# Kernel tuning notes

Hardware: AMD Instinct MI355X
Metric: run time of the kernel (lower is better)

Reference implementation:

```python
import jax, jax.numpy as jnp
import numpy as np

DIM = 1024


def _combine(e1, e2):
    # associative op for h_t = a_t * h_{t-1} + b_t (inclusive scan, h_0-contrib handled outside)
    a1, b1 = e1
    a2, b2 = e2
    return a1 * a2, b2 + a2 * b1


def setup_inputs() -> dict:
    key = jax.random.key(0)
    ks = jax.random.split(key, 11)
    s = 1.0 / np.sqrt(DIM)
    d = {
        "x": jax.random.normal(ks[0], (4, 4096, DIM), jnp.float32),
        "hidden": jax.random.normal(ks[1], (4, DIM), jnp.float32),
        "Wf": jax.random.uniform(ks[2], (DIM, DIM), jnp.float32, -s, s),
        "bf": jax.random.uniform(ks[3], (DIM,), jnp.float32, -s, s),
        "Wi": jax.random.uniform(ks[4], (DIM, DIM), jnp.float32, -s, s),
        "bi": jax.random.uniform(ks[5], (DIM,), jnp.float32, -s, s),
        "Wig": jax.random.uniform(ks[6], (DIM, DIM), jnp.float32, -s, s),
        "big": jax.random.uniform(ks[7], (DIM,), jnp.float32, -s, s),
        "Wog": jax.random.uniform(ks[8], (DIM, DIM), jnp.float32, -s, s),
        "bog": jax.random.uniform(ks[9], (DIM,), jnp.float32, -s, s),
    }
    return d


def reference(x, hidden, Wf, bf, Wi, bi, Wig, big, Wog, bog):
    # x: [B, L, D], hidden: [B, D]
    forget = jax.nn.sigmoid(jnp.einsum("bld,ed->ble", x, Wf) + bf)
    inp = jnp.tanh(jnp.einsum("bld,ed->ble", x, Wi) + bi) * \
          jax.nn.sigmoid(jnp.einsum("bld,ed->ble", x, Wig) + big)
    # parallel scan of h_t = forget_t * h_{t-1} + inp_t with h_0 = 0
    _, h_inner = jax.lax.associative_scan(_combine, (forget, inp), axis=1)
    # add initial-hidden contribution: hidden * prod_{s<=t} forget_s
    h = h_inner + hidden[:, None, :] * jnp.cumprod(forget, axis=1)
    y = jnp.tanh(h) * jax.nn.sigmoid(jnp.einsum("bld,ed->ble", x, Wog) + bog)
    return y, h[:, -1, :]
```

## Files before the change

### kernel.cpp

```cpp
#include <hip/hip_runtime.h>
#include <hip/hip_bf16.h>
#include <cstdint>
#include <cstddef>

#define DIMD 1024
#define LSEQ 4096
#define BATCH 4
#define MTOT (BATCH*LSEQ)
#define NCHUNK 64
#define CHUNKLEN 64
#define GATE_ELEMS ((size_t)MTOT*DIMD)
#define NTILE_K 32

typedef __bf16 bf16x8 __attribute__((ext_vector_type(8)));
typedef float f32x4 __attribute__((ext_vector_type(4)));

__device__ __forceinline__ unsigned short f2bf(float f) {
    union { float f; uint32_t u; } v; v.f = f;
    uint32_t r = v.u + 0x7fffu + ((v.u >> 16) & 1u);
    return (unsigned short)(r >> 16);
}
__device__ __forceinline__ float bits2f(unsigned short b) {
    union { uint32_t u; float f; } v; v.u = ((uint32_t)b) << 16; return v.f;
}
__device__ __forceinline__ float gld(const float* p, size_t o) { return p[o]; }
__device__ __forceinline__ float gld(const unsigned short* p, size_t o) { return bits2f(p[o]); }
__device__ __forceinline__ void  gst(float* p, size_t o, float v) { p[o] = v; }
__device__ __forceinline__ void  gst(unsigned short* p, size_t o, float v) { p[o] = f2bf(v); }

__device__ __forceinline__ float fsig(float x) {
    return __builtin_amdgcn_rcpf(1.f + __expf(-x));
}

__global__ void cast_all(const float* __restrict__ x,
                         const float* __restrict__ Wf, const float* __restrict__ Wi,
                         const float* __restrict__ Wig, const float* __restrict__ Wog,
                         unsigned short* __restrict__ Xb, unsigned short* __restrict__ Wcat) {
    int b = blockIdx.x;
    const float* src; unsigned short* dst; int lb;
    if (b < 8192) { src = x; dst = Xb; lb = b; }
    else {
        int w = (b - 8192) >> 9;
        lb = (b - 8192) & 511;
        src = (w == 0) ? Wf : (w == 1) ? Wi : (w == 2) ? Wig : Wog;
        dst = Wcat + (size_t)w * DIMD * DIMD;
    }
    int i = (lb * 256 + threadIdx.x) * 8;
    float4 a = *(const float4*)(src + i);
    float4 c = *(const float4*)(src + i + 4);
    uint4 o;
    o.x = (uint32_t)f2bf(a.x) | ((uint32_t)f2bf(a.y) << 16);
    o.y = (uint32_t)f2bf(a.z) | ((uint32_t)f2bf(a.w) << 16);
    o.z = (uint32_t)f2bf(c.x) | ((uint32_t)f2bf(c.y) << 16);
    o.w = (uint32_t)f2bf(c.z) | ((uint32_t)f2bf(c.w) << 16);
    *(uint4*)(dst + i) = o;
}

template <typename T>
__global__ __launch_bounds__(512, 4) void gemm_gates_s(
    const unsigned short* __restrict__ Xb,
    const unsigned short* __restrict__ Wcat,
    const float* __restrict__ bf_, const float* __restrict__ bi_,
    const float* __restrict__ big_, const float* __restrict__ bog_,
    T* __restrict__ G)
{
    __shared__ __align__(16) char lds[73728];
    char* ldsA = lds;
    char* ldsB = lds + 24576;

    const int tid = threadIdx.x;
    const int wave = tid >> 6, lane = tid & 63;
    const int wm = wave >> 2, wn = wave & 3;
    const int l15 = lane & 15, l4 = lane >> 4;

    const int wg = blockIdx.x;
    const int swz = (wg & 7) * 256 + (wg >> 3);
    const int mt = swz & 127, nt = swz >> 7;
    const int m0 = mt * 128, n0 = nt * 256;

    const int rsw = (l4 ^ ((l15 >> 1) & 3)) << 4;
    const char* ArdBase = ldsA + (wm * 64 + l15) * 64 + rsw;
    const char* BrdBase = ldsB + (wn * 64 + l15) * 64 + rsw;

    const int srow = tid >> 2;
    const int scg  = ((tid & 3) ^ ((srow >> 1) & 3)) * 8;
    const unsigned short* pAsrc  = Xb   + (size_t)(m0 + srow) * DIMD + scg;
    const unsigned short* pBsrc0 = Wcat + (size_t)(n0 + srow) * DIMD + scg;
    const unsigned short* pBsrc1 = Wcat + (size_t)(n0 + 128 + srow) * DIMD + scg;

    auto stage3 = [&](int k0, int offA, int offB) {
        __builtin_amdgcn_global_load_lds(
            (const __attribute__((address_space(1))) uint32_t*)(pAsrc + k0),
            (__attribute__((address_space(3))) uint32_t*)(ldsA + offA + (wave << 10)), 16, 0, 0);
        __builtin_amdgcn_global_load_lds(
            (const __attribute__((address_space(1))) uint32_t*)(pBsrc0 + k0),
            (__attribute__((address_space(3))) uint32_t*)(ldsB + offB + (wave << 10)), 16, 0, 0);
        __builtin_amdgcn_global_load_lds(
            (const __attribute__((address_space(1))) uint32_t*)(pBsrc1 + k0),
            (__attribute__((address_space(3))) uint32_t*)(ldsB + offB + 8192 + (wave << 10)), 16, 0, 0);
    };

    f32x4 acc[4][4];
#pragma unroll
    for (int m = 0; m < 4; ++m)
#pragma unroll
        for (int n = 0; n < 4; ++n) acc[m][n] = (f32x4)0.f;

    stage3(0, 0, 0);
    stage3(32, 8192, 16384);

    int offA0 = 0, offA1 = 8192, offA2 = 16384;
    int offB0 = 0, offB1 = 16384, offB2 = 32768;
#pragma unroll 1
    for (int t = 0; t < NTILE_K; ++t) {
        if (t <= NTILE_K - 2) asm volatile("s_waitcnt vmcnt(3)" ::: "memory");
        else                  asm volatile("s_waitcnt vmcnt(0)" ::: "memory");
        __builtin_amdgcn_s_barrier();
        __builtin_amdgcn_sched_barrier(0);

        if (t + 2 < NTILE_K) stage3((t + 2) * 32, offA2, offB2);

        bf16x8 bv[4], avl[2], avh[2];
#pragma unroll
        for (int n = 0; n < 4; ++n)
            bv[n] = *(const bf16x8*)(BrdBase + offB0 + n * 1024);
        avl[0] = *(const bf16x8*)(ArdBase + offA0);
        avl[1] = *(const bf16x8*)(ArdBase + offA0 + 1024);

        __builtin_amdgcn_s_setprio(1);
#pragma unroll
        for (int m = 0; m < 2; ++m)
#pragma unroll
            for (int n = 0; n < 4; ++n)
                acc[m][n] = __builtin_amdgcn_mfma_f32_16x16x32_bf16(avl[m], bv[n], acc[m][n], 0, 0, 0);
        __builtin_amdgcn_s_setprio(0);

        avh[0] = *(const bf16x8*)(ArdBase + offA0 + 2048);
        avh[1] = *(const bf16x8*)(ArdBase + offA0 + 3072);

        __builtin_amdgcn_s_setprio(1);
#pragma unroll
        for (int m = 0; m < 2; ++m)
#pragma unroll
            for (int n = 0; n < 4; ++n)
                acc[2 + m][n] = __builtin_amdgcn_mfma_f32_16x16x32_bf16(avh[m], bv[n], acc[2 + m][n], 0, 0, 0);
        __builtin_amdgcn_s_setprio(0);

        int ta = offA0; offA0 = offA1; offA1 = offA2; offA2 = ta;
        int tb = offB0; offB0 = offB1; offB1 = offB2; offB2 = tb;
    }

    const int gate = n0 >> 10;
    const float* bias = (gate == 0) ? bf_ : (gate == 1) ? bi_ : (gate == 2) ? big_ : bog_;
    T* Gg = G + (size_t)gate * GATE_ELEMS;
    const int ebase = (n0 & 1023) + wn * 64;
    const int rowb0 = m0 + wm * 64;
    float bvv[4];
#pragma unroll
    for (int nf = 0; nf < 4; ++nf) bvv[nf] = bias[ebase + nf * 16 + l15];
#pragma unroll
    for (int mf = 0; mf < 4; ++mf) {
        int rowb = rowb0 + mf * 16 + l4 * 4;
#pragma unroll
        for (int r = 0; r < 4; ++r) {
            size_t rowoff = (size_t)(rowb + r) * DIMD;
#pragma unroll
            for (int nf = 0; nf < 4; ++nf) {
                float pre = acc[mf][nf][r] + bvv[nf];
                float v = (gate == 1) ? (2.f * fsig(2.f * pre) - 1.f) : fsig(pre);
                gst(Gg, rowoff + ebase + nf * 16 + l15, v);
            }
        }
    }
}

template <typename T>
__global__ void scan_phase1(const T* __restrict__ F, const T* __restrict__ TI,
                            const T* __restrict__ SG,
                            float* __restrict__ Aagg, float* __restrict__ Bagg) {
    const int d = blockIdx.x * blockDim.x + threadIdx.x;
    const int c = blockIdx.y, b = blockIdx.z;
    size_t base = ((size_t)b * LSEQ + (size_t)c * CHUNKLEN) * DIMD + d;
    float A = 1.f, Bv = 0.f;
#pragma unroll 8
    for (int t = 0; t < CHUNKLEN; ++t) {
        size_t off = base + (size_t)t * DIMD;
        float f = gld(F, off);
        float i = gld(TI, off) * gld(SG, off);
        A *= f;
        Bv = __builtin_fmaf(f, Bv, i);
    }
    size_t o = ((size_t)b * NCHUNK + c) * DIMD + d;
    Aagg[o] = A;
    Bagg[o] = Bv;
}

__global__ void scan_phase2(const float* __restrict__ Aagg, const float* __restrict__ Bagg,
                            const float* __restrict__ hidden,
                            float* __restrict__ Hstart, float* __restrict__ out_h) {
    int idx = blockIdx.x * blockDim.x + threadIdx.x;
    int b = idx >> 10, d = idx & 1023;
    float h = hidden[b * 1024 + d];
    for (int c = 0; c < NCHUNK; ++c) {
        size_t o = ((size_t)b * NCHUNK + c) * DIMD + d;
        Hstart[o] = h;
        h = __builtin_fmaf(Aagg[o], h, Bagg[o]);
    }
    out_h[b * 1024 + d] = h;
}

template <typename T>
__global__ void scan_phase3(const T* __restrict__ F, const T* __restrict__ TI,
                            const T* __restrict__ SG, const T* __restrict__ OG,
                            const float* __restrict__ Hstart, float* __restrict__ y) {
    const int d = blockIdx.x * blockDim.x + threadIdx.x;
    const int c = blockIdx.y, b = blockIdx.z;
    float h = Hstart[((size_t)b * NCHUNK + c) * DIMD + d];
    size_t base = ((size_t)b * LSEQ + (size_t)c * CHUNKLEN) * DIMD + d;
#pragma unroll 4
    for (int t = 0; t < CHUNKLEN; ++t) {
        size_t off = base + (size_t)t * DIMD;
        float f = gld(F, off);
        float i = gld(TI, off) * gld(SG, off);
        h = __builtin_fmaf(f, h, i);
        y[off] = tanhf(h) * gld(OG, off);
    }
}

extern "C" void kernel_launch(void* const* d_in, const int* in_sizes, int n_in,
                              void* d_out, int out_size, void* d_ws, size_t ws_size,
                              hipStream_t stream) {
    const float* x      = (const float*)d_in[0];
    const float* hidden = (const float*)d_in[1];
    const float* Wf  = (const float*)d_in[2];
    const float* bf_ = (const float*)d_in[3];
    const float* Wi  = (const float*)d_in[4];
    const float* bi_ = (const float*)d_in[5];
    const float* Wig = (const float*)d_in[6];
    const float* big_= (const float*)d_in[7];
    const float* Wog = (const float*)d_in[8];
    const float* bog_= (const float*)d_in[9];

    char* ws = (char*)d_ws;
    unsigned short* Xb   = (unsigned short*)(ws);
    unsigned short* Wcat = (unsigned short*)(ws + 33554432);

    float* y     = (float*)d_out;
    float* out_h = y + GATE_ELEMS;

    cast_all<<<10240, 256, 0, stream>>>(x, Wf, Wi, Wig, Wog, Xb, Wcat);

    const int GRID = (MTOT / 128) * (4096 / 256);
    const size_t FP32_WS_NEED = 33554432ull + 8388608ull + GATE_ELEMS * 4 * 4 + 3ull * 1048576ull;
    if (ws_size >= FP32_WS_NEED) {
        float* G      = (float*)(ws + 41943040);
        float* Aagg   = (float*)(ws + 310378496);
        float* Bagg   = (float*)(ws + 311427072);
        float* Hstart = (float*)(ws + 312475648);
        gemm_gates_s<float><<<GRID, 512, 0, stream>>>(Xb, Wcat, bf_, bi_, big_, bog_, G);
        const float* Fg  = G;
        const float* TIg = G + 1 * GATE_ELEMS;
        const float* SGg = G + 2 * GATE_ELEMS;
        const float* OGg = G + 3 * GATE_ELEMS;
        scan_phase1<float><<<dim3(DIMD / 256, NCHUNK, BATCH), 256, 0, stream>>>(Fg, TIg, SGg, Aagg, Bagg);
        scan_phase2<<<BATCH * DIMD / 256, 256, 0, stream>>>(Aagg, Bagg, hidden, Hstart, out_h);
        scan_phase3<float><<<dim3(DIMD / 256, NCHUNK, BATCH), 256, 0, stream>>>(Fg, TIg, SGg, OGg, Hstart, y);
    } else {
        unsigned short* G = (unsigned short*)(ws + 41943040);
        float* Aagg   = (float*)(ws + 176160768);
        float* Bagg   = (float*)(ws + 177209344);
        float* Hstart = (float*)(ws + 178257920);
        gemm_gates_s<unsigned short><<<GRID, 512, 0, stream>>>(Xb, Wcat, bf_, bi_, big_, bog_, G);
        const unsigned short* Fg  = G;
        const unsigned short* TIg = G + 1 * GATE_ELEMS;
        const unsigned short* SGg = G + 2 * GATE_ELEMS;
        const unsigned short* OGg = G + 3 * GATE_ELEMS;
        scan_phase1<unsigned short><<<dim3(DIMD / 256, NCHUNK, BATCH), 256, 0, stream>>>(Fg, TIg, SGg, Aagg, Bagg);
        scan_phase2<<<BATCH * DIMD / 256, 256, 0, stream>>>(Aagg, Bagg, hidden, Hstart, out_h);
        scan_phase3<unsigned short><<<dim3(DIMD / 256, NCHUNK, BATCH), 256, 0, stream>>>(Fg, TIg, SGg, OGg, Hstart, y);
    }
}
```

Measured before the change: 240.4 us.

## Fuse gate activations, input product and chunk scan aggregates into the GEMM epilogue

Each GEMM workgroup's N tile now interleaves the four gates for the same 64 output features, so one block holds forget, tanh-input, input-gate and output-gate values for a 128x64 tile. The epilogue forms the input product, computes per-64-row chunk scan aggregates through LDS and cross-lane shuffles, and writes only F, I and OG in bf16. This removes the scan_phase1 kernel, one full gate tensor write and read, and the fp32 gate path. The epilogue gains serial scan work and LDS traffic, bf16 storage is now always used, and tanhf is replaced by a sigmoid-based approximation.

```diff
diff --git a/kernel.cpp b/kernel.cpp
--- a/kernel.cpp
+++ b/kernel.cpp
@@ -23,13 +23,11 @@
 __device__ __forceinline__ float bits2f(unsigned short b) {
     union { uint32_t u; float f; } v; v.u = ((uint32_t)b) << 16; return v.f;
 }
-__device__ __forceinline__ float gld(const float* p, size_t o) { return p[o]; }
-__device__ __forceinline__ float gld(const unsigned short* p, size_t o) { return bits2f(p[o]); }
-__device__ __forceinline__ void  gst(float* p, size_t o, float v) { p[o] = v; }
-__device__ __forceinline__ void  gst(unsigned short* p, size_t o, float v) { p[o] = f2bf(v); }
-
 __device__ __forceinline__ float fsig(float x) {
     return __builtin_amdgcn_rcpf(1.f + __expf(-x));
+}
+__device__ __forceinline__ float ftanh(float x) {
+    return 2.f * fsig(2.f * x) - 1.f;
 }
 
 __global__ void cast_all(const float* __restrict__ x,
@@ -56,13 +54,14 @@
     *(uint4*)(dst + i) = o;
 }
 
-template <typename T>
-__global__ __launch_bounds__(512, 4) void gemm_gates_s(
+__global__ __launch_bounds__(512, 4) void gemm_gates_f(
     const unsigned short* __restrict__ Xb,
     const unsigned short* __restrict__ Wcat,
     const float* __restrict__ bf_, const float* __restrict__ bi_,
     const float* __restrict__ big_, const float* __restrict__ bog_,
-    T* __restrict__ G)
+    unsigned short* __restrict__ F, unsigned short* __restrict__ I,
+    unsigned short* __restrict__ OG,
+    float* __restrict__ Aagg, float* __restrict__ Bagg)
 {
     __shared__ __align__(16) char lds[73728];
     char* ldsA = lds;
@@ -75,8 +74,8 @@
 
     const int wg = blockIdx.x;
     const int swz = (wg & 7) * 256 + (wg >> 3);
-    const int mt = swz & 127, nt = swz >> 7;
-    const int m0 = mt * 128, n0 = nt * 256;
+    const int mt = swz & 127, et = swz >> 7;
+    const int m0 = mt * 128, e0 = et * 64;
 
     const int rsw = (l4 ^ ((l15 >> 1) & 3)) << 4;
     const char* ArdBase = ldsA + (wm * 64 + l15) * 64 + rsw;
@@ -84,9 +83,9 @@
 
     const int srow = tid >> 2;
     const int scg  = ((tid & 3) ^ ((srow >> 1) & 3)) * 8;
-    const unsigned short* pAsrc  = Xb   + (size_t)(m0 + srow) * DIMD + scg;
-    const unsigned short* pBsrc0 = Wcat + (size_t)(n0 + srow) * DIMD + scg;
-    const unsigned short* pBsrc1 = Wcat + (size_t)(n0 + 128 + srow) * DIMD + scg;
+    const unsigned short* pAsrc = Xb + (size_t)(m0 + srow) * DIMD + scg;
+    const unsigned short* pBsrc0 = Wcat + (size_t)((srow >> 6) * 1024 + e0 + (srow & 63)) * DIMD + scg;
+    const unsigned short* pBsrc1 = Wcat + (size_t)((2 + (srow >> 6)) * 1024 + e0 + (srow & 63)) * DIMD + scg;
 
     auto stage3 = [&](int k0, int offA, int offB) {
         __builtin_amdgcn_global_load_lds(
@@ -150,49 +149,97 @@
         int tb = offB0; offB0 = offB1; offB1 = offB2; offB2 = tb;
     }
 
-    const int gate = n0 >> 10;
-    const float* bias = (gate == 0) ? bf_ : (gate == 1) ? bi_ : (gate == 2) ? big_ : bog_;
-    T* Gg = G + (size_t)gate * GATE_ELEMS;
-    const int ebase = (n0 & 1023) + wn * 64;
-    const int rowb0 = m0 + wm * 64;
+    const float* biasg = (wn == 0) ? bf_ : (wn == 1) ? bi_ : (wn == 2) ? big_ : bog_;
     float bvv[4];
 #pragma unroll
-    for (int nf = 0; nf < 4; ++nf) bvv[nf] = bias[ebase + nf * 16 + l15];
-#pragma unroll
-    for (int mf = 0; mf < 4; ++mf) {
-        int rowb = rowb0 + mf * 16 + l4 * 4;
-#pragma unroll
-        for (int r = 0; r < 4; ++r) {
-            size_t rowoff = (size_t)(rowb + r) * DIMD;
-#pragma unroll
-            for (int nf = 0; nf < 4; ++nf) {
+    for (int nf = 0; nf < 4; ++nf) bvv[nf] = biasg[e0 + nf * 16 + l15];
+
+#pragma unroll
+    for (int mf = 0; mf < 4; ++mf)
+#pragma unroll
+        for (int nf = 0; nf < 4; ++nf)
+#pragma unroll
+            for (int r = 0; r < 4; ++r) {
                 float pre = acc[mf][nf][r] + bvv[nf];
-                float v = (gate == 1) ? (2.f * fsig(2.f * pre) - 1.f) : fsig(pre);
-                gst(Gg, rowoff + ebase + nf * 16 + l15, v);
+                acc[mf][nf][r] = (wn == 1) ? ftanh(pre) : fsig(pre);
+            }
+
+    float* ldsF  = (float*)lds;
+    float* ldsSG = (float*)(lds + 32768);
+    __builtin_amdgcn_s_barrier();
+    if (wn == 0 || wn == 2) {
+        float* dstL = (wn == 0 ? ldsF : ldsSG) + wm * 4096;
+#pragma unroll
+        for (int mf = 0; mf < 4; ++mf)
+#pragma unroll
+            for (int nf = 0; nf < 4; ++nf)
+#pragma unroll
+                for (int r = 0; r < 4; ++r)
+                    dstL[(mf * 16 + l4 * 4 + r) * 64 + nf * 16 + l15] = acc[mf][nf][r];
+    }
+    __builtin_amdgcn_s_barrier();
+
+    const size_t rowbase = (size_t)(m0 + wm * 64) * DIMD + e0;
+    if (wn == 0) {
+#pragma unroll
+        for (int mf = 0; mf < 4; ++mf)
+#pragma unroll
+            for (int r = 0; r < 4; ++r) {
+                size_t ro = rowbase + (size_t)(mf * 16 + l4 * 4 + r) * DIMD;
+#pragma unroll
+                for (int nf = 0; nf < 4; ++nf)
+                    F[ro + nf * 16 + l15] = f2bf(acc[mf][nf][r]);
+            }
+    } else if (wn == 3) {
+#pragma unroll
+        for (int mf = 0; mf < 4; ++mf)
+#pragma unroll
+            for (int r = 0; r < 4; ++r) {
+                size_t ro = rowbase + (size_t)(mf * 16 + l4 * 4 + r) * DIMD;
+#pragma unroll
+                for (int nf = 0; nf < 4; ++nf)
+                    OG[ro + nf * 16 + l15] = f2bf(acc[mf][nf][r]);
+            }
+    } else if (wn == 1) {
+        const float* fL  = ldsF  + wm * 4096;
+        const float* sgL = ldsSG + wm * 4096;
+        const int gc = (m0 >> 6) + wm;
+#pragma unroll
+        for (int nf = 0; nf < 4; ++nf) {
+            float A = 1.f, Bv = 0.f;
+#pragma unroll
+            for (int mf = 0; mf < 4; ++mf) {
+                float sA = 1.f, sB = 0.f;
+#pragma unroll
+                for (int r = 0; r < 4; ++r) {
+                    int row = mf * 16 + l4 * 4 + r;
+                    int ecl = nf * 16 + l15;
+                    float fv = fL[row * 64 + ecl];
+                    float iv = acc[mf][nf][r] * sgL[row * 64 + ecl];
+                    I[rowbase + (size_t)row * DIMD + ecl] = f2bf(iv);
+                    sA = fv * sA;
+                    sB = __builtin_fmaf(fv, sB, iv);
+                }
+#pragma unroll
+                for (int s = 16; s <= 32; s <<= 1) {
+                    float Ap = __shfl_xor(sA, s, 64);
+                    float Bp = __shfl_xor(sB, s, 64);
+                    bool later = (lane & s) != 0;
+                    float aE = later ? Ap : sA, bE = later ? Bp : sB;
+                    float aL = later ? sA : Ap, bL = later ? sB : Bp;
+                    sA = aE * aL;
+                    sB = __builtin_fmaf(aL, bE, bL);
+                }
+                Bv = __builtin_fmaf(sA, Bv, sB);
+                A  = A * sA;
+            }
+            if (l4 == 0) {
+                int e = e0 + nf * 16 + l15;
+                Aagg[(size_t)gc * DIMD + e] = A;
+                Bagg[(size_t)gc * DIMD + e] = Bv;
             }
         }
     }
-}
-
-template <typename T>
-__global__ void scan_phase1(const T* __restrict__ F, const T* __restrict__ TI,
-                            const T* __restrict__ SG,
-                            float* __restrict__ Aagg, float* __restrict__ Bagg) {
-    const int d = blockIdx.x * blockDim.x + threadIdx.x;
-    const int c = blockIdx.y, b = blockIdx.z;
-    size_t base = ((size_t)b * LSEQ + (size_t)c * CHUNKLEN) * DIMD + d;
-    float A = 1.f, Bv = 0.f;
-#pragma unroll 8
-    for (int t = 0; t < CHUNKLEN; ++t) {
-        size_t off = base + (size_t)t * DIMD;
-        float f = gld(F, off);
-        float i = gld(TI, off) * gld(SG, off);
-        A *= f;
-        Bv = __builtin_fmaf(f, Bv, i);
-    }
-    size_t o = ((size_t)b * NCHUNK + c) * DIMD + d;
-    Aagg[o] = A;
-    Bagg[o] = Bv;
 }
 
 __global__ void scan_phase2(const float* __restrict__ Aagg, const float* __restrict__ Bagg,
@@ -209,9 +256,9 @@
     out_h[b * 1024 + d] = h;
 }
 
-template <typename T>
-__global__ void scan_phase3(const T* __restrict__ F, const T* __restrict__ TI,
-                            const T* __restrict__ SG, const T* __restrict__ OG,
+__global__ void scan_phase3(const unsigned short* __restrict__ F,
+                            const unsigned short* __restrict__ I,
+                            const unsigned short* __restrict__ OG,
                             const float* __restrict__ Hstart, float* __restrict__ y) {
     const int d = blockIdx.x * blockDim.x + threadIdx.x;
     const int c = blockIdx.y, b = blockIdx.z;
@@ -220,10 +267,8 @@
 #pragma unroll 4
     for (int t = 0; t < CHUNKLEN; ++t) {
         size_t off = base + (size_t)t * DIMD;
-        float f = gld(F, off);
-        float i = gld(TI, off) * gld(SG, off);
-        h = __builtin_fmaf(f, h, i);
-        y[off] = tanhf(h) * gld(OG, off);
+        h = __builtin_fmaf(bits2f(F[off]), h, bits2f(I[off]));
+        y[off] = ftanh(h) * bits2f(OG[off]);
     }
 }
 
@@ -244,39 +289,21 @@
     char* ws = (char*)d_ws;
     unsigned short* Xb   = (unsigned short*)(ws);
     unsigned short* Wcat = (unsigned short*)(ws + 33554432);
+    unsigned short* F    = (unsigned short*)(ws + 41943040);
+    unsigned short* I    = (unsigned short*)(ws + 75497472);
+    unsigned short* OG   = (unsigned short*)(ws + 109051904);
+    float* Aagg   = (float*)(ws + 142606336);
+    float* Bagg   = (float*)(ws + 143654912);
+    float* Hstart = (float*)(ws + 144703488);
 
     float* y     = (float*)d_out;
     float* out_h = y + GATE_ELEMS;
 
     cast_all<<<10240, 256, 0, stream>>>(x, Wf, Wi, Wig, Wog, Xb, Wcat);
 
-    const int GRID = (MTOT / 128) * (4096 / 256);
-    const size_t FP32_WS_NEED = 33554432ull + 8388608ull + GATE_ELEMS * 4 * 4 + 3ull * 1048576ull;
-    if (ws_size >= FP32_WS_NEED) {
-        float* G      = (float*)(ws + 41943040);
-        float* Aagg   = (float*)(ws + 310378496);
-        float* Bagg   = (float*)(ws + 311427072);
-        float* Hstart = (float*)(ws + 312475648);
-        gemm_gates_s<float><<<GRID, 512, 0, stream>>>(Xb, Wcat, bf_, bi_, big_, bog_, G);
-        const float* Fg  = G;
-        const float* TIg = G + 1 * GATE_ELEMS;
-        const float* SGg = G + 2 * GATE_ELEMS;
-        const float* OGg = G + 3 * GATE_ELEMS;
-        scan_phase1<float><<<dim3(DIMD / 256, NCHUNK, BATCH), 256, 0, stream>>>(Fg, TIg, SGg, Aagg, Bagg);
-        scan_phase2<<<BATCH * DIMD / 256, 256, 0, stream>>>(Aagg, Bagg, hidden, Hstart, out_h);
-        scan_phase3<float><<<dim3(DIMD / 256, NCHUNK, BATCH), 256, 0, stream>>>(Fg, TIg, SGg, OGg, Hstart, y);
-    } else {
-        unsigned short* G = (unsigned short*)(ws + 41943040);
-        float* Aagg   = (float*)(ws + 176160768);
-        float* Bagg   = (float*)(ws + 177209344);
-        float* Hstart = (float*)(ws + 178257920);
-        gemm_gates_s<unsigned short><<<GRID, 512, 0, stream>>>(Xb, Wcat, bf_, bi_, big_, bog_, G);
-        const unsigned short* Fg  = G;
-        const unsigned short* TIg = G + 1 * GATE_ELEMS;
-        const unsigned short* SGg = G + 2 * GATE_ELEMS;
-        const unsigned short* OGg = G + 3 * GATE_ELEMS;
-        scan_phase1<unsigned short><<<dim3(DIMD / 256, NCHUNK, BATCH), 256, 0, stream>>>(Fg, TIg, SGg, Aagg, Bagg);
-        scan_phase2<<<BATCH * DIMD / 256, 256, 0, stream>>>(Aagg, Bagg, hidden, Hstart, out_h);
-        scan_phase3<unsigned short><<<dim3(DIMD / 256, NCHUNK, BATCH), 256, 0, stream>>>(Fg, TIg, SGg, OGg, Hstart, y);
-    }
-}
+    gemm_gates_f<<<2048, 512, 0, stream>>>(Xb, Wcat, bf_, bi_, big_, bog_,
+                                           F, I, OG, Aagg, Bagg);
+
+    scan_phase2<<<BATCH * DIMD / 256, 256, 0, stream>>>(Aagg, Bagg, hidden, Hstart, out_h);
+    scan_phase3<<<dim3(DIMD / 256, NCHUNK, BATCH), 256, 0, stream>>>(F, I, OG, Hstart, y);
+}
```

New measurement: 226.1 us. 1.06x faster.
